# Optimization experiments

Measured on AMD Instinct MI355X. Metric: run time of the kernel, lower is better.

Reference implementation:

```python
import jax, jax.numpy as jnp
import numpy as np

NK_DIM = 64
EK_DIM = 16
TEMPERATURE = 8.0
NEG_INF = -1e9


def setup_inputs() -> dict:
    key = jax.random.key(0)
    k1, k2, k3, k4, k5 = jax.random.split(key, 5)
    B, H, N, DV = 4, 8, 256, 64
    q = jax.random.normal(k1, (B, H, N, NK_DIM + EK_DIM), dtype=jnp.float32)
    nk = jax.random.normal(k2, (B, H, N, NK_DIM), dtype=jnp.float32)
    ek = jax.random.normal(k3, (B, H, N, N, EK_DIM), dtype=jnp.float32)
    v = jax.random.normal(k4, (B, H, N, DV), dtype=jnp.float32)
    mask = jax.random.randint(k5, (B, 1, N, N), 0, 2, dtype=jnp.int32)
    return {"q": q, "nk": nk, "ek": ek, "v": v, "mask": mask}


def reference(q, nk, ek, v, mask):
    # split query into node part and edge part
    qn = q[..., :NK_DIM]   # [B,H,N,nk]
    qe = q[..., NK_DIM:]   # [B,H,N,ek]
    # standard scaled dot-product term: [B,H,N,N]
    node_attn = jnp.einsum('bhqd,bhkd->bhqk', qn, nk)
    # per-edge key term: contract qe against 5D edge keys -> [B,H,N,N]
    edge_attn = jnp.einsum('bhqd,bhqkd->bhqk', qe, ek)
    attn = (node_attn + edge_attn) / TEMPERATURE
    attn = jnp.where(mask == 0, jnp.asarray(NEG_INF, attn.dtype), attn)
    attn = jax.nn.softmax(attn, axis=-1)
    # dropout p=0.0 (identity) in this reference
    output = jnp.einsum('bhqk,bhkd->bhqd', attn, v)
    return output, attn
```

## Files before the change

### kernel.cpp

```cpp
#include <hip/hip_runtime.h>

constexpr int NKD = 64;
constexpr int EKD = 16;
constexpr int QD  = 80;
constexpr int NN  = 256;
constexpr int DVD = 64;
constexpr int BB  = 4;
constexpr int HH  = 8;
constexpr int QT  = 16;
constexpr int NT  = 256;

__global__ __launch_bounds__(256) void sdpe_kernel(
    const float* __restrict__ q, const float* __restrict__ nk,
    const float* __restrict__ ek, const float* __restrict__ v,
    const int* __restrict__ mask, float* __restrict__ out, float* __restrict__ attn_out)
{
    const int bid  = blockIdx.x;
    const int bh   = bid >> 4;
    const int q0   = (bid & 15) * QT;
    const int b    = bh >> 3;
    const int tid  = threadIdx.x;
    const int wave = tid >> 6;
    const int lane = tid & 63;

    __shared__ float s_q[QT * QD];
    __shared__ float s_S[QT * NN];

    {
        const float4* qsrc = (const float4*)(q + ((size_t)bh * NN + q0) * QD);
        float4*       qdst = (float4*)s_q;
        for (int i = tid; i < QT * QD / 4; i += NT) qdst[i] = qsrc[i];
    }

    float4 nkr[16];
    {
        const float4* nkp = (const float4*)(nk + ((size_t)bh * NN + tid) * NKD);
        #pragma unroll
        for (int j = 0; j < 16; ++j) nkr[j] = nkp[j];
    }
    __syncthreads();

    #pragma unroll
    for (int r = 0; r < QT; ++r) {
        const size_t rowg = (size_t)bh * NN + q0 + r;
        const float4* qr  = (const float4*)(s_q + r * QD);
        float acc = 0.f;
        #pragma unroll
        for (int j = 0; j < 16; ++j) {
            const float4 a = qr[j], n = nkr[j];
            acc += a.x * n.x + a.y * n.y + a.z * n.z + a.w * n.w;
        }
        const float4* ekp = (const float4*)(ek + (rowg * NN + tid) * EKD);
        #pragma unroll
        for (int j = 0; j < 4; ++j) {
            const float4 a = qr[16 + j], e = ekp[j];
            acc += a.x * e.x + a.y * e.y + a.z * e.z + a.w * e.w;
        }
        acc *= 0.125f;
        if (mask[((size_t)b * NN + q0 + r) * NN + tid] == 0) acc = -1.0e9f;
        s_S[r * NN + tid] = acc;
    }
    __syncthreads();

    #pragma unroll
    for (int rr = 0; rr < 4; ++rr) {
        const int r = wave * 4 + rr;
        float4 f = *(const float4*)&s_S[r * NN + lane * 4];
        float mx = fmaxf(fmaxf(f.x, f.y), fmaxf(f.z, f.w));
        #pragma unroll
        for (int o = 32; o >= 1; o >>= 1) mx = fmaxf(mx, __shfl_xor(mx, o));
        float4 e;
        e.x = __expf(f.x - mx); e.y = __expf(f.y - mx);
        e.z = __expf(f.z - mx); e.w = __expf(f.w - mx);
        float s = e.x + e.y + e.z + e.w;
        #pragma unroll
        for (int o = 32; o >= 1; o >>= 1) s += __shfl_xor(s, o);
        const float inv = 1.f / s;
        e.x *= inv; e.y *= inv; e.z *= inv; e.w *= inv;
        *(float4*)&s_S[r * NN + lane * 4] = e;
        const size_t rowg = (size_t)bh * NN + q0 + r;
        *(float4*)(attn_out + rowg * NN + lane * 4) = e;
    }
    __syncthreads();

    const int d4 = lane & 15;
    const int kg = lane >> 4;
    const int r0 = wave * 4;
    float4 acc[4];
    #pragma unroll
    for (int rr = 0; rr < 4; ++rr) acc[rr] = make_float4(0.f, 0.f, 0.f, 0.f);

    const float* vb = v + (size_t)bh * NN * DVD + d4 * 4;
    #pragma unroll 4
    for (int k = kg; k < NN; k += 4) {
        const float4 v4 = *(const float4*)(vb + (size_t)k * DVD);
        #pragma unroll
        for (int rr = 0; rr < 4; ++rr) {
            const float a = s_S[(r0 + rr) * NN + k];
            acc[rr].x += a * v4.x; acc[rr].y += a * v4.y;
            acc[rr].z += a * v4.z; acc[rr].w += a * v4.w;
        }
    }
    #pragma unroll
    for (int rr = 0; rr < 4; ++rr) {
        acc[rr].x += __shfl_xor(acc[rr].x, 16);
        acc[rr].y += __shfl_xor(acc[rr].y, 16);
        acc[rr].z += __shfl_xor(acc[rr].z, 16);
        acc[rr].w += __shfl_xor(acc[rr].w, 16);
        acc[rr].x += __shfl_xor(acc[rr].x, 32);
        acc[rr].y += __shfl_xor(acc[rr].y, 32);
        acc[rr].z += __shfl_xor(acc[rr].z, 32);
        acc[rr].w += __shfl_xor(acc[rr].w, 32);
    }
    if (kg == 0) {
        #pragma unroll
        for (int rr = 0; rr < 4; ++rr) {
            const size_t rowg = (size_t)bh * NN + q0 + r0 + rr;
            *(float4*)(out + rowg * DVD + d4 * 4) = acc[rr];
        }
    }
}

extern "C" void kernel_launch(void* const* d_in, const int* in_sizes, int n_in,
                              void* d_out, int out_size, void* d_ws, size_t ws_size,
                              hipStream_t stream) {
    const float* q    = (const float*)d_in[0];
    const float* nk   = (const float*)d_in[1];
    const float* ek   = (const float*)d_in[2];
    const float* v    = (const float*)d_in[3];
    const int*   mask = (const int*)d_in[4];

    float* out      = (float*)d_out;
    float* attn_out = out + (size_t)BB * HH * NN * DVD;

    const int nblocks = BB * HH * (NN / QT);
    sdpe_kernel<<<nblocks, NT, 0, stream>>>(q, nk, ek, v, mask, out, attn_out);
}
```

Measured before the change: 214.0 us.

## Halve query tile, coalesce edge-key loads, stage node keys in swizzled LDS

The query tile shrinks from 16 to 8 rows, doubling the block count, and launch bounds now request 4 blocks per SM. Edge-key loads become fully coalesced float4 reads where each group of 4 lanes reduces one key's 16-wide dot product with shuffles. The node-key term is computed from 64-row tiles of nk staged in XOR-swizzled shared memory instead of 64 floats held per thread in registers, and the mask is applied later with vectorised int4 loads. The PV loop reads 4 attention weights per float4. The goal is better DRAM efficiency on the dominant ek stream and higher occupancy, at the cost of more barriers and nk being reloaded by twice as many blocks.

```diff
diff --git a/kernel.cpp b/kernel.cpp
--- a/kernel.cpp
+++ b/kernel.cpp
@@ -7,17 +7,17 @@
 constexpr int DVD = 64;
 constexpr int BB  = 4;
 constexpr int HH  = 8;
-constexpr int QT  = 16;
+constexpr int QT  = 8;
 constexpr int NT  = 256;
 
-__global__ __launch_bounds__(256) void sdpe_kernel(
+__global__ __launch_bounds__(256, 4) void sdpe_kernel(
     const float* __restrict__ q, const float* __restrict__ nk,
     const float* __restrict__ ek, const float* __restrict__ v,
     const int* __restrict__ mask, float* __restrict__ out, float* __restrict__ attn_out)
 {
     const int bid  = blockIdx.x;
-    const int bh   = bid >> 4;
-    const int q0   = (bid & 15) * QT;
+    const int bh   = bid >> 5;
+    const int q0   = (bid & 31) * QT;
     const int b    = bh >> 3;
     const int tid  = threadIdx.x;
     const int wave = tid >> 6;
@@ -25,47 +25,75 @@
 
     __shared__ float s_q[QT * QD];
     __shared__ float s_S[QT * NN];
+    __shared__ float s_nk[64 * 64];
 
     {
-        const float4* qsrc = (const float4*)(q + ((size_t)bh * NN + q0) * QD);
-        float4*       qdst = (float4*)s_q;
-        for (int i = tid; i < QT * QD / 4; i += NT) qdst[i] = qsrc[i];
-    }
-
-    float4 nkr[16];
-    {
-        const float4* nkp = (const float4*)(nk + ((size_t)bh * NN + tid) * NKD);
-        #pragma unroll
-        for (int j = 0; j < 16; ++j) nkr[j] = nkp[j];
+        const float4* src = (const float4*)(q + ((size_t)bh * NN + q0) * QD);
+        if (tid < QT * QD / 4) ((float4*)s_q)[tid] = src[tid];
     }
     __syncthreads();
 
-    #pragma unroll
-    for (int r = 0; r < QT; ++r) {
-        const size_t rowg = (size_t)bh * NN + q0 + r;
-        const float4* qr  = (const float4*)(s_q + r * QD);
-        float acc = 0.f;
-        #pragma unroll
-        for (int j = 0; j < 16; ++j) {
-            const float4 a = qr[j], n = nkr[j];
-            acc += a.x * n.x + a.y * n.y + a.z * n.z + a.w * n.w;
+    {
+        const int jb = tid & 3;
+        const int kb = tid >> 2;
+        const float4* ekb = (const float4*)ek + ((size_t)bh * NN + q0) * (NN * EKD / 4);
+        #pragma unroll 2
+        for (int r = 0; r < QT; ++r) {
+            const float4 qe4 = *(const float4*)&s_q[r * QD + NKD + jb * 4];
+            const float4 e0 = ekb[(size_t)r * 1024 + tid];
+            const float4 e1 = ekb[(size_t)r * 1024 + tid + 256];
+            const float4 e2 = ekb[(size_t)r * 1024 + tid + 512];
+            const float4 e3 = ekb[(size_t)r * 1024 + tid + 768];
+            float p0 = e0.x*qe4.x + e0.y*qe4.y + e0.z*qe4.z + e0.w*qe4.w;
+            float p1 = e1.x*qe4.x + e1.y*qe4.y + e1.z*qe4.z + e1.w*qe4.w;
+            float p2 = e2.x*qe4.x + e2.y*qe4.y + e2.z*qe4.z + e2.w*qe4.w;
+            float p3 = e3.x*qe4.x + e3.y*qe4.y + e3.z*qe4.z + e3.w*qe4.w;
+            p0 += __shfl_xor(p0, 1);  p0 += __shfl_xor(p0, 2);
+            p1 += __shfl_xor(p1, 1);  p1 += __shfl_xor(p1, 2);
+            p2 += __shfl_xor(p2, 1);  p2 += __shfl_xor(p2, 2);
+            p3 += __shfl_xor(p3, 1);  p3 += __shfl_xor(p3, 2);
+            const float pw = (jb == 0) ? p0 : (jb == 1) ? p1 : (jb == 2) ? p2 : p3;
+            s_S[r * NN + kb + 64 * jb] = pw;
         }
-        const float4* ekp = (const float4*)(ek + (rowg * NN + tid) * EKD);
-        #pragma unroll
-        for (int j = 0; j < 4; ++j) {
-            const float4 a = qr[16 + j], e = ekp[j];
-            acc += a.x * e.x + a.y * e.y + a.z * e.z + a.w * e.w;
-        }
-        acc *= 0.125f;
-        if (mask[((size_t)b * NN + q0 + r) * NN + tid] == 0) acc = -1.0e9f;
-        s_S[r * NN + tid] = acc;
     }
     __syncthreads();
 
+    for (int kt = 0; kt < 4; ++kt) {
+        {
+            const float4* src = (const float4*)nk + ((size_t)bh * NN + kt * 64) * (NKD / 4);
+            #pragma unroll
+            for (int i = 0; i < 4; ++i) {
+                const int f   = tid + 256 * i;
+                const int row = f >> 4, c4 = f & 15;
+                *(float4*)&s_nk[row * 64 + ((c4 ^ (row & 7)) << 2)] = src[f];
+            }
+        }
+        __syncthreads();
+        float acc0 = 0.f, acc1 = 0.f;
+        #pragma unroll
+        for (int j4 = 0; j4 < 16; ++j4) {
+            const float4 n4 = *(const float4*)&s_nk[lane * 64 + ((j4 ^ (lane & 7)) << 2)];
+            const float4 qa = *(const float4*)&s_q[wave * QD + j4 * 4];
+            const float4 qb = *(const float4*)&s_q[(wave + 4) * QD + j4 * 4];
+            acc0 += n4.x*qa.x + n4.y*qa.y + n4.z*qa.z + n4.w*qa.w;
+            acc1 += n4.x*qb.x + n4.y*qb.y + n4.z*qb.z + n4.w*qb.w;
+        }
+        const int kg = kt * 64 + lane;
+        s_S[wave * NN + kg]       += acc0;
+        s_S[(wave + 4) * NN + kg] += acc1;
+        __syncthreads();
+    }
+
     #pragma unroll
-    for (int rr = 0; rr < 4; ++rr) {
-        const int r = wave * 4 + rr;
+    for (int rr = 0; rr < 2; ++rr) {
+        const int r = wave + rr * 4;
+        const size_t rowg = (size_t)bh * NN + q0 + r;
         float4 f = *(const float4*)&s_S[r * NN + lane * 4];
+        const int4 m4 = *(const int4*)(mask + ((size_t)b * NN + q0 + r) * NN + lane * 4);
+        f.x = (m4.x == 0) ? -1e9f : f.x * 0.125f;
+        f.y = (m4.y == 0) ? -1e9f : f.y * 0.125f;
+        f.z = (m4.z == 0) ? -1e9f : f.z * 0.125f;
+        f.w = (m4.w == 0) ? -1e9f : f.w * 0.125f;
         float mx = fmaxf(fmaxf(f.x, f.y), fmaxf(f.z, f.w));
         #pragma unroll
         for (int o = 32; o >= 1; o >>= 1) mx = fmaxf(mx, __shfl_xor(mx, o));
@@ -78,45 +106,45 @@
         const float inv = 1.f / s;
         e.x *= inv; e.y *= inv; e.z *= inv; e.w *= inv;
         *(float4*)&s_S[r * NN + lane * 4] = e;
-        const size_t rowg = (size_t)bh * NN + q0 + r;
         *(float4*)(attn_out + rowg * NN + lane * 4) = e;
     }
     __syncthreads();
 
-    const int d4 = lane & 15;
-    const int kg = lane >> 4;
-    const int r0 = wave * 4;
-    float4 acc[4];
-    #pragma unroll
-    for (int rr = 0; rr < 4; ++rr) acc[rr] = make_float4(0.f, 0.f, 0.f, 0.f);
-
-    const float* vb = v + (size_t)bh * NN * DVD + d4 * 4;
-    #pragma unroll 4
-    for (int k = kg; k < NN; k += 4) {
-        const float4 v4 = *(const float4*)(vb + (size_t)k * DVD);
-        #pragma unroll
-        for (int rr = 0; rr < 4; ++rr) {
-            const float a = s_S[(r0 + rr) * NN + k];
-            acc[rr].x += a * v4.x; acc[rr].y += a * v4.y;
-            acc[rr].z += a * v4.z; acc[rr].w += a * v4.w;
+    {
+        const int d4 = lane & 15;
+        const int kq = lane >> 4;
+        float4 a0 = make_float4(0.f,0.f,0.f,0.f), a1 = make_float4(0.f,0.f,0.f,0.f);
+        const float* vb = v + (size_t)bh * NN * DVD + d4 * 4;
+        #pragma unroll 4
+        for (int i = 0; i < 16; ++i) {
+            const int k0 = i * 16 + kq * 4;
+            const float4 w0 = *(const float4*)&s_S[wave * NN + k0];
+            const float4 w1 = *(const float4*)&s_S[(wave + 4) * NN + k0];
+            const float4 v0 = *(const float4*)(vb + (size_t)(k0 + 0) * DVD);
+            const float4 v1 = *(const float4*)(vb + (size_t)(k0 + 1) * DVD);
+            const float4 v2 = *(const float4*)(vb + (size_t)(k0 + 2) * DVD);
+            const float4 v3 = *(const float4*)(vb + (size_t)(k0 + 3) * DVD);
+            a0.x += w0.x*v0.x + w0.y*v1.x + w0.z*v2.x + w0.w*v3.x;
+            a0.y += w0.x*v0.y + w0.y*v1.y + w0.z*v2.y + w0.w*v3.y;
+            a0.z += w0.x*v0.z + w0.y*v1.z + w0.z*v2.z + w0.w*v3.z;
+            a0.w += w0.x*v0.w + w0.y*v1.w + w0.z*v2.w + w0.w*v3.w;
+            a1.x += w1.x*v0.x + w1.y*v1.x + w1.z*v2.x + w1.w*v3.x;
+            a1.y += w1.x*v0.y + w1.y*v1.y + w1.z*v2.y + w1.w*v3.y;
+            a1.z += w1.x*v0.z + w1.y*v1.z + w1.z*v2.z + w1.w*v3.z;
+            a1.w += w1.x*v0.w + w1.y*v1.w + w1.z*v2.w + w1.w*v3.w;
         }
-    }
-    #pragma unroll
-    for (int rr = 0; rr < 4; ++rr) {
-        acc[rr].x += __shfl_xor(acc[rr].x, 16);
-        acc[rr].y += __shfl_xor(acc[rr].y, 16);
-        acc[rr].z += __shfl_xor(acc[rr].z, 16);
-        acc[rr].w += __shfl_xor(acc[rr].w, 16);
-        acc[rr].x += __shfl_xor(acc[rr].x, 32);
-        acc[rr].y += __shfl_xor(acc[rr].y, 32);
-        acc[rr].z += __shfl_xor(acc[rr].z, 32);
-        acc[rr].w += __shfl_xor(acc[rr].w, 32);
-    }
-    if (kg == 0) {
-        #pragma unroll
-        for (int rr = 0; rr < 4; ++rr) {
-            const size_t rowg = (size_t)bh * NN + q0 + r0 + rr;
-            *(float4*)(out + rowg * DVD + d4 * 4) = acc[rr];
+        a0.x += __shfl_xor(a0.x, 16); a0.y += __shfl_xor(a0.y, 16);
+        a0.z += __shfl_xor(a0.z, 16); a0.w += __shfl_xor(a0.w, 16);
+        a1.x += __shfl_xor(a1.x, 16); a1.y += __shfl_xor(a1.y, 16);
+        a1.z += __shfl_xor(a1.z, 16); a1.w += __shfl_xor(a1.w, 16);
+        a0.x += __shfl_xor(a0.x, 32); a0.y += __shfl_xor(a0.y, 32);
+        a0.z += __shfl_xor(a0.z, 32); a0.w += __shfl_xor(a0.w, 32);
+        a1.x += __shfl_xor(a1.x, 32); a1.y += __shfl_xor(a1.y, 32);
+        a1.z += __shfl_xor(a1.z, 32); a1.w += __shfl_xor(a1.w, 32);
+        if (kq == 0) {
+            const size_t rowg0 = (size_t)bh * NN + q0 + wave;
+            *(float4*)(out + rowg0 * DVD + d4 * 4)       = a0;
+            *(float4*)(out + (rowg0 + 4) * DVD + d4 * 4) = a1;
         }
     }
 }
```

New measurement: 220.9 us. 1.03x slower.
